# Kernel optimization log

Hardware: AMD Instinct MI355X
Metric: run time of the kernel (lower is better)

## Reference

```python
import jax, jax.numpy as jnp
import numpy as np

N_NODES = 70000
N_EDGES = 800000
IN_SAGE = 1024
FEAT_CH = 128
EXTRA = 20
HIDDEN = (FEAT_CH + EXTRA) // 4  # 37
OUT = 3
BN_EPS = 1e-5


def setup_inputs() -> dict:
    key = jax.random.key(0)
    ks = jax.random.split(key, 12)
    features = jax.random.normal(ks[0], (N_NODES, 1044), dtype=jnp.float32)
    edges = jax.random.randint(ks[1], (2, N_EDGES), 0, N_NODES, dtype=jnp.int32)
    edges2 = jax.random.randint(ks[2], (2, N_EDGES), 0, N_NODES, dtype=jnp.int32)
    edge_features = jax.random.normal(ks[3], (N_EDGES, 1), dtype=jnp.float32)
    s = 1.0 / np.sqrt(IN_SAGE)
    w_sage_l = jax.random.uniform(ks[4], (FEAT_CH, IN_SAGE), jnp.float32, -s, s)
    b_sage_l = jax.random.uniform(ks[5], (FEAT_CH,), jnp.float32, -s, s)
    w_sage_r = jax.random.uniform(ks[6], (FEAT_CH, IN_SAGE), jnp.float32, -s, s)
    s1 = 1.0 / np.sqrt(FEAT_CH + EXTRA)
    fc1_w = jax.random.uniform(ks[7], (HIDDEN, FEAT_CH + EXTRA), jnp.float32, -s1, s1)
    fc1_b = jax.random.uniform(ks[8], (HIDDEN,), jnp.float32, -s1, s1)
    s2 = 1.0 / np.sqrt(HIDDEN)
    fc2_w = jax.random.uniform(ks[9], (OUT, HIDDEN), jnp.float32, -s2, s2)
    fc2_b = jax.random.uniform(ks[10], (OUT,), jnp.float32, -s2, s2)
    bn_gamma = jnp.ones((HIDDEN,), jnp.float32)
    bn_beta = jnp.zeros((HIDDEN,), jnp.float32)
    bn_mean = jnp.zeros((HIDDEN,), jnp.float32)
    bn_var = jnp.ones((HIDDEN,), jnp.float32)
    return dict(features=features, edges=edges, edges2=edges2, edge_features=edge_features,
                w_sage_l=w_sage_l, b_sage_l=b_sage_l, w_sage_r=w_sage_r,
                fc1_w=fc1_w, fc1_b=fc1_b, fc2_w=fc2_w, fc2_b=fc2_b,
                bn_gamma=bn_gamma, bn_beta=bn_beta, bn_mean=bn_mean, bn_var=bn_var)


def reference(features, edges, edges2, edge_features,
              w_sage_l, b_sage_l, w_sage_r,
              fc1_w, fc1_b, fc2_w, fc2_b,
              bn_gamma, bn_beta, bn_mean, bn_var):
    n = features.shape[0]
    x_in = features[:, :IN_SAGE]            # [N, 1024]
    src, dst = edges[0], edges[1]
    # SAGEConv mean aggregation: mean of source-node features per destination node
    agg = jax.ops.segment_sum(x_in[src], dst, num_segments=n)          # [N, 1024]
    cnt = jax.ops.segment_sum(jnp.ones_like(dst, jnp.float32), dst, num_segments=n)
    mean = agg / jnp.maximum(cnt, 1.0)[:, None]
    # lin_l(aggr) + lin_r(x)  (PyG SAGEConv, root_weight=True, bias on lin_l)
    x = mean @ w_sage_l.T + b_sage_l + x_in @ w_sage_r.T               # [N, 128]
    x = jax.nn.relu(x)                                                 # activation; dropout is identity in eval
    x = jnp.concatenate([x, features[:, IN_SAGE:]], axis=1)            # [N, 148]
    x = jax.nn.relu(x @ fc1_w.T + fc1_b)                               # [N, 37]
    x = (x - bn_mean) * jax.lax.rsqrt(bn_var + BN_EPS) * bn_gamma + bn_beta  # BatchNorm1d eval
    return x @ fc2_w.T + fc2_b                                         # [N, 3]
```

## Files before the change

kernel.cpp:

```cpp
#include <hip/hip_runtime.h>
#include <hip/hip_bf16.h>

#define N_NODES 70000
#define N_EDGES 800000
#define ROWLEN  1044
#define KDIM    1024
#define FEAT    128
#define NOUT    256
#define HIDDEN  37
#define CIN     148
#define NCHUNK  69
#define TM      96

typedef __attribute__((ext_vector_type(8))) short short8;
typedef __attribute__((ext_vector_type(4))) float f32x4;

static __device__ __forceinline__ unsigned short f2bf(float f) {
  unsigned int u = __float_as_uint(f);
  u += 0x7FFF + ((u >> 16) & 1);
  return (unsigned short)(u >> 16);
}
static __device__ __forceinline__ float bf2f(unsigned int u) {
  return __uint_as_float(u << 16);
}
static __device__ __forceinline__ unsigned int pk2bf(float a, float b) {
  union { __hip_bfloat162 h; unsigned int u; } cv;
  cv.h = __float22bfloat162_rn(float2{a, b});
  return cv.u;
}

__global__ __launch_bounds__(256) void cvt_w(
    const float* __restrict__ wl, const float* __restrict__ wr,
    unsigned short* __restrict__ wbf, unsigned int* __restrict__ z)
{
  const int i = blockIdx.x * 256 + threadIdx.x;
  const int half = (FEAT * KDIM) / 4;
  const float* src = (i < half) ? wl : wr;
  const int j = (i < half) ? i : (i - half);
  const float4 v = ((const float4*)src)[j];
  uint2 u = make_uint2(pk2bf(v.x, v.y), pk2bf(v.z, v.w));
  ((uint2*)wbf)[i] = u;
  for (int k = i; k < 2 * N_NODES; k += 65536) z[k] = 0u;
}

__global__ __launch_bounds__(256) void hist(
    const int* __restrict__ edges, unsigned int* __restrict__ cnt)
{
  const int e = blockIdx.x * 256 + threadIdx.x;
  atomicAdd(&cnt[edges[N_EDGES + e]], 1u);
}

__global__ __launch_bounds__(256) void scan_a(
    const unsigned int* __restrict__ cnt, unsigned int* __restrict__ partial)
{
  __shared__ unsigned int s[256];
  const int t = threadIdx.x;
  const int base = blockIdx.x * 1024 + t * 4;
  unsigned int sum = 0;
  #pragma unroll
  for (int j = 0; j < 4; j++) sum += (base + j < N_NODES) ? cnt[base + j] : 0u;
  s[t] = sum; __syncthreads();
  for (int off = 128; off > 0; off >>= 1) {
    if (t < off) s[t] += s[t + off];
    __syncthreads();
  }
  if (t == 0) partial[blockIdx.x] = s[0];
}

__global__ __launch_bounds__(128) void scan_b(
    const unsigned int* __restrict__ partial, unsigned int* __restrict__ chunk_off)
{
  __shared__ unsigned int s[128];
  const int t = threadIdx.x;
  const unsigned int own = (t < NCHUNK) ? partial[t] : 0u;
  s[t] = own; __syncthreads();
  for (int off = 1; off < 128; off <<= 1) {
    unsigned int x = (t >= off) ? s[t - off] : 0u;
    __syncthreads();
    s[t] += x;
    __syncthreads();
  }
  if (t < NCHUNK) chunk_off[t] = s[t] - own;
}

__global__ __launch_bounds__(256) void scan_c(
    const unsigned int* __restrict__ cnt, const unsigned int* __restrict__ chunk_off,
    unsigned int* __restrict__ row_start)
{
  __shared__ unsigned int s[256];
  const int t = threadIdx.x;
  const int base = blockIdx.x * 1024 + t * 4;
  unsigned int v[4], sum = 0;
  #pragma unroll
  for (int j = 0; j < 4; j++) { v[j] = (base + j < N_NODES) ? cnt[base + j] : 0u; sum += v[j]; }
  s[t] = sum; __syncthreads();
  for (int off = 1; off < 256; off <<= 1) {
    unsigned int x = (t >= off) ? s[t - off] : 0u;
    __syncthreads();
    s[t] += x;
    __syncthreads();
  }
  unsigned int run = chunk_off[blockIdx.x] + (s[t] - sum);
  #pragma unroll
  for (int j = 0; j < 4; j++) {
    if (base + j < N_NODES) row_start[base + j] = run;
    run += v[j];
  }
}

__global__ __launch_bounds__(256) void fill_csr(
    const int* __restrict__ edges, const unsigned int* __restrict__ row_start,
    unsigned int* __restrict__ wc, int* __restrict__ col)
{
  const int e = blockIdx.x * 256 + threadIdx.x;
  const int src = edges[e];
  const int dst = edges[N_EDGES + e];
  const unsigned int pos = row_start[dst] + atomicAdd(&wc[dst], 1u);
  col[pos] = src;
}

__global__ __launch_bounds__(256, 3) void gemm_sage(
    const float* __restrict__ feat,
    const unsigned short* __restrict__ wbf,
    unsigned short* __restrict__ y)
{
  __shared__ __align__(16) unsigned short As[TM][72];
  __shared__ __align__(16) unsigned short Bs[256][72];

  const int tid  = threadIdx.x;
  const int lane = tid & 63;
  const int wid  = tid >> 6;
  const int wm   = (wid & 1) * 48;
  const int wn   = (wid >> 1) * 128;
  const int m0   = blockIdx.x * TM;

  f32x4 acc[3][8];
  const f32x4 zero = {0.f, 0.f, 0.f, 0.f};
  #pragma unroll
  for (int i = 0; i < 3; i++)
    #pragma unroll
    for (int j = 0; j < 8; j++) acc[i][j] = zero;

  const int c4  = tid & 15;
  const int r0  = tid >> 4;
  const int c8  = tid & 7;
  const int r0b = tid >> 3;

  for (int kk = 0; kk < KDIM; kk += 64) {
    #pragma unroll
    for (int i = 0; i < 6; i++) {
      int r = r0 + 16 * i;
      int m = m0 + r; if (m >= N_NODES) m = N_NODES - 1;
      const float4 v = *(const float4*)(feat + (size_t)m * ROWLEN + kk + c4 * 4);
      uint2 u = make_uint2(pk2bf(v.x, v.y), pk2bf(v.z, v.w));
      *(uint2*)&As[r][c4 * 4] = u;
    }
    #pragma unroll
    for (int i = 0; i < 8; i++) {
      int r = r0b + 32 * i;
      const uint4 v = *(const uint4*)(wbf + (size_t)r * KDIM + kk + c8 * 8);
      *(uint4*)&Bs[r][c8 * 8] = v;
    }
    __syncthreads();
    #pragma unroll
    for (int s = 0; s < 2; s++) {
      const int colk = s * 32 + (lane >> 4) * 8;
      const int row  = lane & 15;
      short8 a[3];
      #pragma unroll
      for (int t = 0; t < 3; t++) a[t] = *(const short8*)&As[wm + t * 16 + row][colk];
      #pragma unroll
      for (int j = 0; j < 8; j++) {
        const short8 b = *(const short8*)&Bs[wn + j * 16 + row][colk];
        #pragma unroll
        for (int t = 0; t < 3; t++)
          acc[t][j] = __builtin_amdgcn_mfma_f32_16x16x32_bf16(a[t], b, acc[t][j], 0, 0, 0);
      }
    }
    __syncthreads();
  }

  const int mb = m0 + wm + (lane >> 4) * 4;
  const int nb = wn + (lane & 15);
  #pragma unroll
  for (int t = 0; t < 3; t++) {
    #pragma unroll
    for (int r = 0; r < 4; r++) {
      const int m = mb + t * 16 + r;
      if (m < N_NODES) {
        #pragma unroll
        for (int j = 0; j < 8; j++)
          y[(size_t)m * NOUT + nb + j * 16] = f2bf(acc[t][j][r]);
      }
    }
  }
}

__global__ __launch_bounds__(256) void gather_epilogue(
    const float* __restrict__ feat,
    const unsigned short* __restrict__ y,
    const unsigned int* __restrict__ row_start,
    const unsigned int* __restrict__ cnt,
    const int* __restrict__ col,
    const float* __restrict__ b_sage_l,
    const float* __restrict__ fc1_w, const float* __restrict__ fc1_b,
    const float* __restrict__ fc2_w, const float* __restrict__ fc2_b,
    const float* __restrict__ bn_gamma, const float* __restrict__ bn_beta,
    const float* __restrict__ bn_mean, const float* __restrict__ bn_var,
    float* __restrict__ out)
{
  __shared__ float w1t[CIN][HIDDEN + 1];
  __shared__ float vbuf[4][CIN];
  __shared__ float hbuf[4][HIDDEN + 3];
  const int tid  = threadIdx.x;
  const int lane = tid & 63;
  const int w    = tid >> 6;

  for (int i = tid; i < HIDDEN * CIN; i += 256) {
    const int j = i / CIN;
    const int c = i - j * CIN;
    w1t[c][j] = fc1_w[i];
  }
  __syncthreads();

  const int m = blockIdx.x * 4 + w;
  const int e0 = (int)row_start[m];
  const int n  = (int)cnt[m];

  float s0 = 0.f, s1 = 0.f;
  int i = 0;
  for (; i + 4 <= n; i += 4) {
    const int sa = col[e0 + i];
    const int sb = col[e0 + i + 1];
    const int sc = col[e0 + i + 2];
    const int sd = col[e0 + i + 3];
    const unsigned int va = *(const unsigned int*)(y + (size_t)sa * NOUT + lane * 2);
    const unsigned int vb = *(const unsigned int*)(y + (size_t)sb * NOUT + lane * 2);
    const unsigned int vc = *(const unsigned int*)(y + (size_t)sc * NOUT + lane * 2);
    const unsigned int vd = *(const unsigned int*)(y + (size_t)sd * NOUT + lane * 2);
    s0 += (bf2f(va & 0xFFFFu) + bf2f(vb & 0xFFFFu)) + (bf2f(vc & 0xFFFFu) + bf2f(vd & 0xFFFFu));
    s1 += (bf2f(va >> 16)     + bf2f(vb >> 16))     + (bf2f(vc >> 16)     + bf2f(vd >> 16));
  }
  for (; i < n; i++) {
    const int sa = col[e0 + i];
    const unsigned int va = *(const unsigned int*)(y + (size_t)sa * NOUT + lane * 2);
    s0 += bf2f(va & 0xFFFFu);
    s1 += bf2f(va >> 16);
  }

  const float inv = 1.0f / fmaxf((float)n, 1.0f);
  const unsigned int vr = *(const unsigned int*)(y + (size_t)m * NOUT + FEAT + lane * 2);
  vbuf[w][2 * lane]     = fmaxf(s0 * inv + b_sage_l[2 * lane]     + bf2f(vr & 0xFFFFu), 0.0f);
  vbuf[w][2 * lane + 1] = fmaxf(s1 * inv + b_sage_l[2 * lane + 1] + bf2f(vr >> 16),     0.0f);
  if (lane < CIN - FEAT)
    vbuf[w][FEAT + lane] = feat[(size_t)m * ROWLEN + KDIM + lane];
  __syncthreads();

  if (lane < HIDDEN) {
    float h = fc1_b[lane];
    #pragma unroll 4
    for (int c = 0; c < CIN; c++) h += w1t[c][lane] * vbuf[w][c];
    h = fmaxf(h, 0.0f);
    h = (h - bn_mean[lane]) * rsqrtf(bn_var[lane] + 1e-5f) * bn_gamma[lane] + bn_beta[lane];
    hbuf[w][lane] = h;
  }
  __syncthreads();

  if (lane < 3) {
    float o = fc2_b[lane];
    #pragma unroll
    for (int j = 0; j < HIDDEN; j++) o += fc2_w[lane * HIDDEN + j] * hbuf[w][j];
    out[(size_t)m * 3 + lane] = o;
  }
}

#define Y_OFF    0u
#define Y_BYTES  (N_NODES * NOUT * 2u)
#define WBF_OFF  Y_BYTES
#define WBF_BYTES (NOUT * KDIM * 2u)
#define CNT_OFF  (WBF_OFF + WBF_BYTES)
#define CNT_BYTES (N_NODES * 4u)
#define WC_OFF   (CNT_OFF + CNT_BYTES)
#define RS_OFF   (WC_OFF + CNT_BYTES)
#define PART_OFF (RS_OFF + CNT_BYTES)
#define COFF_OFF (PART_OFF + 512u)
#define COL_OFF  (COFF_OFF + 512u)
#define COL_BYTES (N_EDGES * 4u)

extern "C" void kernel_launch(void* const* d_in, const int* in_sizes, int n_in,
                              void* d_out, int out_size, void* d_ws, size_t ws_size,
                              hipStream_t stream) {
  const float* feat     = (const float*)d_in[0];
  const int*   edges    = (const int*)  d_in[1];
  const float* w_sage_l = (const float*)d_in[4];
  const float* b_sage_l = (const float*)d_in[5];
  const float* w_sage_r = (const float*)d_in[6];
  const float* fc1_w    = (const float*)d_in[7];
  const float* fc1_b    = (const float*)d_in[8];
  const float* fc2_w    = (const float*)d_in[9];
  const float* fc2_b    = (const float*)d_in[10];
  const float* bn_gamma = (const float*)d_in[11];
  const float* bn_beta  = (const float*)d_in[12];
  const float* bn_mean  = (const float*)d_in[13];
  const float* bn_var   = (const float*)d_in[14];
  float* out = (float*)d_out;

  char* ws = (char*)d_ws;
  unsigned short* y    = (unsigned short*)(ws + Y_OFF);
  unsigned short* wbf  = (unsigned short*)(ws + WBF_OFF);
  unsigned int*   cnt  = (unsigned int*)(ws + CNT_OFF);
  unsigned int*   wc   = (unsigned int*)(ws + WC_OFF);
  unsigned int*   rs   = (unsigned int*)(ws + RS_OFF);
  unsigned int*   part = (unsigned int*)(ws + PART_OFF);
  unsigned int*   coff = (unsigned int*)(ws + COFF_OFF);
  int*            col  = (int*)(ws + COL_OFF);

  cvt_w<<<256, 256, 0, stream>>>(w_sage_l, w_sage_r, wbf, cnt);
  hist<<<N_EDGES / 256, 256, 0, stream>>>(edges, cnt);
  scan_a<<<NCHUNK, 256, 0, stream>>>(cnt, part);
  scan_b<<<1, 128, 0, stream>>>(part, coff);
  scan_c<<<NCHUNK, 256, 0, stream>>>(cnt, coff, rs);
  fill_csr<<<N_EDGES / 256, 256, 0, stream>>>(edges, rs, wc, col);
  gemm_sage<<<(N_NODES + TM - 1) / TM, 256, 0, stream>>>(feat, wbf, y);
  gather_epilogue<<<N_NODES / 4, 256, 0, stream>>>(feat, y, rs, cnt, col, b_sage_l,
                                                   fc1_w, fc1_b, fc2_w, fc2_b,
                                                   bn_gamma, bn_beta, bn_mean, bn_var, out);
}
```

Before: 683.9 us.

## Use direct-to-LDS swizzled weight loads, single-kernel scan, slot-based CSR fill, wider gather

The GEMM now loads the bf16 weight tile with global_load_lds directly into LDS using an XOR swizzle, in place of register staging into a padded array. The three-kernel scan is replaced by a single-block scan over a padded count array. The CSR fill reuses the per-edge slot returned by the histogram atomics, dropping the second atomic pass. The gather epilogue processes 16 nodes per block, with two half-waves each reading 4 channels per edge and combining through a shuffle. The fused design adds more workspace for slots, and the single-block scan serializes that step.

```diff
diff --git a/kernel.cpp b/kernel.cpp
--- a/kernel.cpp
+++ b/kernel.cpp
@@ -2,6 +2,7 @@
 #include <hip/hip_bf16.h>
 
 #define N_NODES 70000
+#define N_PAD   70656
 #define N_EDGES 800000
 #define ROWLEN  1044
 #define KDIM    1024
@@ -9,7 +10,6 @@
 #define NOUT    256
 #define HIDDEN  37
 #define CIN     148
-#define NCHUNK  69
 #define TM      96
 
 typedef __attribute__((ext_vector_type(8))) short short8;
@@ -27,6 +27,11 @@
   union { __hip_bfloat162 h; unsigned int u; } cv;
   cv.h = __float22bfloat162_rn(float2{a, b});
   return cv.u;
+}
+static __device__ __forceinline__ void load_lds16(const void* g, void* l) {
+  __builtin_amdgcn_global_load_lds(
+      (const __attribute__((address_space(1))) unsigned int*)g,
+      (__attribute__((address_space(3))) unsigned int*)l, 16, 0, 0);
 }
 
 __global__ __launch_bounds__(256) void cvt_w(
@@ -40,83 +45,54 @@
   const float4 v = ((const float4*)src)[j];
   uint2 u = make_uint2(pk2bf(v.x, v.y), pk2bf(v.z, v.w));
   ((uint2*)wbf)[i] = u;
-  for (int k = i; k < 2 * N_NODES; k += 65536) z[k] = 0u;
+  for (int k = i; k < N_PAD; k += 65536) z[k] = 0u;
 }
 
 __global__ __launch_bounds__(256) void hist(
-    const int* __restrict__ edges, unsigned int* __restrict__ cnt)
+    const int* __restrict__ edges, unsigned int* __restrict__ cnt,
+    unsigned int* __restrict__ slot)
 {
   const int e = blockIdx.x * 256 + threadIdx.x;
-  atomicAdd(&cnt[edges[N_EDGES + e]], 1u);
-}
-
-__global__ __launch_bounds__(256) void scan_a(
-    const unsigned int* __restrict__ cnt, unsigned int* __restrict__ partial)
+  slot[e] = atomicAdd(&cnt[edges[N_EDGES + e]], 1u);
+}
+
+__global__ __launch_bounds__(256) void scan_all(
+    const unsigned int* __restrict__ cnt, unsigned int* __restrict__ rs)
 {
   __shared__ unsigned int s[256];
   const int t = threadIdx.x;
-  const int base = blockIdx.x * 1024 + t * 4;
+  const int base = t * 276;
   unsigned int sum = 0;
-  #pragma unroll
-  for (int j = 0; j < 4; j++) sum += (base + j < N_NODES) ? cnt[base + j] : 0u;
+  for (int j = 0; j < 276; j += 4) {
+    const uint4 v = *(const uint4*)(cnt + base + j);
+    sum += v.x + v.y + v.z + v.w;
+  }
+  const unsigned int own = sum;
   s[t] = sum; __syncthreads();
-  for (int off = 128; off > 0; off >>= 1) {
-    if (t < off) s[t] += s[t + off];
-    __syncthreads();
-  }
-  if (t == 0) partial[blockIdx.x] = s[0];
-}
-
-__global__ __launch_bounds__(128) void scan_b(
-    const unsigned int* __restrict__ partial, unsigned int* __restrict__ chunk_off)
-{
-  __shared__ unsigned int s[128];
-  const int t = threadIdx.x;
-  const unsigned int own = (t < NCHUNK) ? partial[t] : 0u;
-  s[t] = own; __syncthreads();
-  for (int off = 1; off < 128; off <<= 1) {
-    unsigned int x = (t >= off) ? s[t - off] : 0u;
+  for (int off = 1; off < 256; off <<= 1) {
+    const unsigned int x = (t >= off) ? s[t - off] : 0u;
     __syncthreads();
     s[t] += x;
     __syncthreads();
   }
-  if (t < NCHUNK) chunk_off[t] = s[t] - own;
-}
-
-__global__ __launch_bounds__(256) void scan_c(
-    const unsigned int* __restrict__ cnt, const unsigned int* __restrict__ chunk_off,
-    unsigned int* __restrict__ row_start)
-{
-  __shared__ unsigned int s[256];
-  const int t = threadIdx.x;
-  const int base = blockIdx.x * 1024 + t * 4;
-  unsigned int v[4], sum = 0;
-  #pragma unroll
-  for (int j = 0; j < 4; j++) { v[j] = (base + j < N_NODES) ? cnt[base + j] : 0u; sum += v[j]; }
-  s[t] = sum; __syncthreads();
-  for (int off = 1; off < 256; off <<= 1) {
-    unsigned int x = (t >= off) ? s[t - off] : 0u;
-    __syncthreads();
-    s[t] += x;
-    __syncthreads();
-  }
-  unsigned int run = chunk_off[blockIdx.x] + (s[t] - sum);
-  #pragma unroll
-  for (int j = 0; j < 4; j++) {
-    if (base + j < N_NODES) row_start[base + j] = run;
-    run += v[j];
+  unsigned int run = s[t] - own;
+  for (int j = 0; j < 276; j += 4) {
+    const uint4 v = *(const uint4*)(cnt + base + j);
+    uint4 o;
+    o.x = run; run += v.x;
+    o.y = run; run += v.y;
+    o.z = run; run += v.z;
+    o.w = run; run += v.w;
+    *(uint4*)(rs + base + j) = o;
   }
 }
 
 __global__ __launch_bounds__(256) void fill_csr(
-    const int* __restrict__ edges, const unsigned int* __restrict__ row_start,
-    unsigned int* __restrict__ wc, int* __restrict__ col)
+    const int* __restrict__ edges, const unsigned int* __restrict__ rs,
+    const unsigned int* __restrict__ slot, int* __restrict__ col)
 {
   const int e = blockIdx.x * 256 + threadIdx.x;
-  const int src = edges[e];
-  const int dst = edges[N_EDGES + e];
-  const unsigned int pos = row_start[dst] + atomicAdd(&wc[dst], 1u);
-  col[pos] = src;
+  col[rs[edges[N_EDGES + e]] + slot[e]] = edges[e];
 }
 
 __global__ __launch_bounds__(256, 3) void gemm_sage(
@@ -125,7 +101,7 @@
     unsigned short* __restrict__ y)
 {
   __shared__ __align__(16) unsigned short As[TM][72];
-  __shared__ __align__(16) unsigned short Bs[256][72];
+  __shared__ __align__(16) unsigned short Bs[256 * 64];
 
   const int tid  = threadIdx.x;
   const int lane = tid & 63;
@@ -141,10 +117,11 @@
     #pragma unroll
     for (int j = 0; j < 8; j++) acc[i][j] = zero;
 
-  const int c4  = tid & 15;
-  const int r0  = tid >> 4;
-  const int c8  = tid & 7;
-  const int r0b = tid >> 3;
+  const int c4    = tid & 15;
+  const int r0    = tid >> 4;
+  const int rbase = wid * 64;
+  const int bs    = lane & 7;
+  const int brow  = lane >> 3;
 
   for (int kk = 0; kk < KDIM; kk += 64) {
     #pragma unroll
@@ -157,9 +134,10 @@
     }
     #pragma unroll
     for (int i = 0; i < 8; i++) {
-      int r = r0b + 32 * i;
-      const uint4 v = *(const uint4*)(wbf + (size_t)r * KDIM + kk + c8 * 8);
-      *(uint4*)&Bs[r][c8 * 8] = v;
+      const int n   = rbase + i * 8 + brow;
+      const int c16 = bs ^ (n & 7);
+      load_lds16(wbf + (size_t)n * KDIM + kk + c16 * 8,
+                 &Bs[(rbase + i * 8) * 64]);
     }
     __syncthreads();
     #pragma unroll
@@ -171,7 +149,8 @@
       for (int t = 0; t < 3; t++) a[t] = *(const short8*)&As[wm + t * 16 + row][colk];
       #pragma unroll
       for (int j = 0; j < 8; j++) {
-        const short8 b = *(const short8*)&Bs[wn + j * 16 + row][colk];
+        const int nr = wn + j * 16 + row;
+        const short8 b = *(const short8*)&Bs[nr * 64 + (((colk >> 3) ^ (nr & 7)) * 8)];
         #pragma unroll
         for (int t = 0; t < 3; t++)
           acc[t][j] = __builtin_amdgcn_mfma_f32_16x16x32_bf16(a[t], b, acc[t][j], 0, 0, 0);
@@ -199,7 +178,7 @@
 __global__ __launch_bounds__(256) void gather_epilogue(
     const float* __restrict__ feat,
     const unsigned short* __restrict__ y,
-    const unsigned int* __restrict__ row_start,
+    const unsigned int* __restrict__ rs,
     const unsigned int* __restrict__ cnt,
     const int* __restrict__ col,
     const float* __restrict__ b_sage_l,
@@ -223,54 +202,55 @@
   }
   __syncthreads();
 
-  const int m = blockIdx.x * 4 + w;
-  const int e0 = (int)row_start[m];
-  const int n  = (int)cnt[m];
-
-  float s0 = 0.f, s1 = 0.f;
-  int i = 0;
-  for (; i + 4 <= n; i += 4) {
-    const int sa = col[e0 + i];
-    const int sb = col[e0 + i + 1];
-    const int sc = col[e0 + i + 2];
-    const int sd = col[e0 + i + 3];
-    const unsigned int va = *(const unsigned int*)(y + (size_t)sa * NOUT + lane * 2);
-    const unsigned int vb = *(const unsigned int*)(y + (size_t)sb * NOUT + lane * 2);
-    const unsigned int vc = *(const unsigned int*)(y + (size_t)sc * NOUT + lane * 2);
-    const unsigned int vd = *(const unsigned int*)(y + (size_t)sd * NOUT + lane * 2);
-    s0 += (bf2f(va & 0xFFFFu) + bf2f(vb & 0xFFFFu)) + (bf2f(vc & 0xFFFFu) + bf2f(vd & 0xFFFFu));
-    s1 += (bf2f(va >> 16)     + bf2f(vb >> 16))     + (bf2f(vc >> 16)     + bf2f(vd >> 16));
-  }
-  for (; i < n; i++) {
-    const int sa = col[e0 + i];
-    const unsigned int va = *(const unsigned int*)(y + (size_t)sa * NOUT + lane * 2);
-    s0 += bf2f(va & 0xFFFFu);
-    s1 += bf2f(va >> 16);
-  }
-
-  const float inv = 1.0f / fmaxf((float)n, 1.0f);
-  const unsigned int vr = *(const unsigned int*)(y + (size_t)m * NOUT + FEAT + lane * 2);
-  vbuf[w][2 * lane]     = fmaxf(s0 * inv + b_sage_l[2 * lane]     + bf2f(vr & 0xFFFFu), 0.0f);
-  vbuf[w][2 * lane + 1] = fmaxf(s1 * inv + b_sage_l[2 * lane + 1] + bf2f(vr >> 16),     0.0f);
-  if (lane < CIN - FEAT)
-    vbuf[w][FEAT + lane] = feat[(size_t)m * ROWLEN + KDIM + lane];
-  __syncthreads();
-
-  if (lane < HIDDEN) {
-    float h = fc1_b[lane];
-    #pragma unroll 4
-    for (int c = 0; c < CIN; c++) h += w1t[c][lane] * vbuf[w][c];
-    h = fmaxf(h, 0.0f);
-    h = (h - bn_mean[lane]) * rsqrtf(bn_var[lane] + 1e-5f) * bn_gamma[lane] + bn_beta[lane];
-    hbuf[w][lane] = h;
-  }
-  __syncthreads();
-
-  if (lane < 3) {
-    float o = fc2_b[lane];
-    #pragma unroll
-    for (int j = 0; j < HIDDEN; j++) o += fc2_w[lane * HIDDEN + j] * hbuf[w][j];
-    out[(size_t)m * 3 + lane] = o;
+  const int sub = lane >> 5;
+  const int ch4 = lane & 31;
+
+  #pragma unroll
+  for (int rep = 0; rep < 4; rep++) {
+    const int m  = blockIdx.x * 16 + w * 4 + rep;
+    const int e0 = (int)rs[m];
+    const int n  = (int)cnt[m];
+
+    float s0 = 0.f, s1 = 0.f, s2 = 0.f, s3 = 0.f;
+    for (int i = 0; i < n; i += 2) {
+      const int idx = i + sub;
+      const bool act = idx < n;
+      const int sa = col[e0 + (act ? idx : i)];
+      const uint2 v = *(const uint2*)(y + (size_t)sa * NOUT + ch4 * 4);
+      if (act) {
+        s0 += bf2f(v.x & 0xFFFFu); s1 += bf2f(v.x >> 16);
+        s2 += bf2f(v.y & 0xFFFFu); s3 += bf2f(v.y >> 16);
+      }
+    }
+    s0 += __shfl_xor(s0, 32); s1 += __shfl_xor(s1, 32);
+    s2 += __shfl_xor(s2, 32); s3 += __shfl_xor(s3, 32);
+
+    const float inv = 1.0f / fmaxf((float)n, 1.0f);
+    if (lane < 32) {
+      const uint2 vr = *(const uint2*)(y + (size_t)m * NOUT + FEAT + ch4 * 4);
+      const int c0 = ch4 * 4;
+      vbuf[w][c0 + 0] = fmaxf(s0 * inv + b_sage_l[c0 + 0] + bf2f(vr.x & 0xFFFFu), 0.f);
+      vbuf[w][c0 + 1] = fmaxf(s1 * inv + b_sage_l[c0 + 1] + bf2f(vr.x >> 16),     0.f);
+      vbuf[w][c0 + 2] = fmaxf(s2 * inv + b_sage_l[c0 + 2] + bf2f(vr.y & 0xFFFFu), 0.f);
+      vbuf[w][c0 + 3] = fmaxf(s3 * inv + b_sage_l[c0 + 3] + bf2f(vr.y >> 16),     0.f);
+    }
+    if (lane < CIN - FEAT)
+      vbuf[w][FEAT + lane] = feat[(size_t)m * ROWLEN + KDIM + lane];
+
+    if (lane < HIDDEN) {
+      float h = fc1_b[lane];
+      #pragma unroll 4
+      for (int c = 0; c < CIN; c++) h += w1t[c][lane] * vbuf[w][c];
+      h = fmaxf(h, 0.0f);
+      h = (h - bn_mean[lane]) * rsqrtf(bn_var[lane] + 1e-5f) * bn_gamma[lane] + bn_beta[lane];
+      hbuf[w][lane] = h;
+    }
+    if (lane < 3) {
+      float o = fc2_b[lane];
+      #pragma unroll
+      for (int j = 0; j < HIDDEN; j++) o += fc2_w[lane * HIDDEN + j] * hbuf[w][j];
+      out[(size_t)m * 3 + lane] = o;
+    }
   }
 }
 
@@ -279,13 +259,11 @@
 #define WBF_OFF  Y_BYTES
 #define WBF_BYTES (NOUT * KDIM * 2u)
 #define CNT_OFF  (WBF_OFF + WBF_BYTES)
-#define CNT_BYTES (N_NODES * 4u)
-#define WC_OFF   (CNT_OFF + CNT_BYTES)
-#define RS_OFF   (WC_OFF + CNT_BYTES)
-#define PART_OFF (RS_OFF + CNT_BYTES)
-#define COFF_OFF (PART_OFF + 512u)
-#define COL_OFF  (COFF_OFF + 512u)
-#define COL_BYTES (N_EDGES * 4u)
+#define CNT_BYTES (N_PAD * 4u)
+#define RS_OFF   (CNT_OFF + CNT_BYTES)
+#define SLOT_OFF (RS_OFF + CNT_BYTES)
+#define SLOT_BYTES (N_EDGES * 4u)
+#define COL_OFF  (SLOT_OFF + SLOT_BYTES)
 
 extern "C" void kernel_launch(void* const* d_in, const int* in_sizes, int n_in,
                               void* d_out, int out_size, void* d_ws, size_t ws_size,
@@ -309,20 +287,16 @@
   unsigned short* y    = (unsigned short*)(ws + Y_OFF);
   unsigned short* wbf  = (unsigned short*)(ws + WBF_OFF);
   unsigned int*   cnt  = (unsigned int*)(ws + CNT_OFF);
-  unsigned int*   wc   = (unsigned int*)(ws + WC_OFF);
   unsigned int*   rs   = (unsigned int*)(ws + RS_OFF);
-  unsigned int*   part = (unsigned int*)(ws + PART_OFF);
-  unsigned int*   coff = (unsigned int*)(ws + COFF_OFF);
+  unsigned int*   slot = (unsigned int*)(ws + SLOT_OFF);
   int*            col  = (int*)(ws + COL_OFF);
 
   cvt_w<<<256, 256, 0, stream>>>(w_sage_l, w_sage_r, wbf, cnt);
-  hist<<<N_EDGES / 256, 256, 0, stream>>>(edges, cnt);
-  scan_a<<<NCHUNK, 256, 0, stream>>>(cnt, part);
-  scan_b<<<1, 128, 0, stream>>>(part, coff);
-  scan_c<<<NCHUNK, 256, 0, stream>>>(cnt, coff, rs);
-  fill_csr<<<N_EDGES / 256, 256, 0, stream>>>(edges, rs, wc, col);
+  hist<<<N_EDGES / 256, 256, 0, stream>>>(edges, cnt, slot);
+  scan_all<<<1, 256, 0, stream>>>(cnt, rs);
+  fill_csr<<<N_EDGES / 256, 256, 0, stream>>>(edges, rs, slot, col);
   gemm_sage<<<(N_NODES + TM - 1) / TM, 256, 0, stream>>>(feat, wbf, y);
-  gather_epilogue<<<N_NODES / 4, 256, 0, stream>>>(feat, y, rs, cnt, col, b_sage_l,
-                                                   fc1_w, fc1_b, fc2_w, fc2_b,
-                                                   bn_gamma, bn_beta, bn_mean, bn_var, out);
-}
+  gather_epilogue<<<N_NODES / 16, 256, 0, stream>>>(feat, y, rs, cnt, col, b_sage_l,
+                                                    fc1_w, fc1_b, fc2_w, fc2_b,
+                                                    bn_gamma, bn_beta, bn_mean, bn_var, out);
+}
```

Measured after the change: 709.2 us. +3.7%, slower.
